# Kernel tuning notes

Hardware: AMD Instinct MI355X
Metric: run time of the kernel (lower is better)

Reference implementation:

```python
import jax, jax.numpy as jnp
import numpy as np

B, S, H, NH = 4, 2048, 1024, 16
D = H // NH  # head_dim = 64


def setup_inputs() -> dict:
    key = jax.random.key(0)
    ks = jax.random.split(key, 8)
    hidden_states = jax.random.normal(ks[0], (B, S, H), dtype=jnp.float32)
    attention_mask = jnp.zeros((B, 1, 1, S), dtype=jnp.float32)  # additive, bidirectional
    # RoPE tables (cos/sin per position, full head_dim)
    inv_freq = 1.0 / (10000.0 ** (jnp.arange(0, D, 2, dtype=jnp.float32) / D))
    t = jnp.arange(S, dtype=jnp.float32)
    freqs = jnp.outer(t, inv_freq)              # [S, D/2]
    emb = jnp.concatenate([freqs, freqs], -1)   # [S, D]
    cos, sin = jnp.cos(emb), jnp.sin(emb)
    scale = 1.0 / np.sqrt(H)
    Wq = jax.random.normal(ks[1], (H, H), dtype=jnp.float32) * scale
    Wk = jax.random.normal(ks[2], (H, H), dtype=jnp.float32) * scale
    Wv = jax.random.normal(ks[3], (H, H), dtype=jnp.float32) * scale
    Wo = jax.random.normal(ks[4], (H, H), dtype=jnp.float32) * scale
    return {"hidden_states": hidden_states, "attention_mask": attention_mask,
            "cos": cos, "sin": sin, "Wq": Wq, "Wk": Wk, "Wv": Wv, "Wo": Wo}


def _rotate_half(x):
    x1, x2 = jnp.split(x, 2, axis=-1)
    return jnp.concatenate([-x2, x1], axis=-1)


def _rope(x, cos, sin):
    # x: [B, NH, S, D]; cos/sin: [S, D]
    c = cos[None, None, :, :]
    s = sin[None, None, :, :]
    return x * c + _rotate_half(x) * s


def reference(hidden_states, attention_mask, cos, sin, Wq, Wk, Wv, Wo):
    b, s, h = hidden_states.shape
    # QKV projections (torch Linear: x @ W^T)
    def proj(W):
        y = jnp.einsum('bsh,oh->bso', hidden_states, W)
        return y.reshape(b, s, NH, D).transpose(0, 2, 1, 3)  # [B, NH, S, D]
    q, k, v = proj(Wq), proj(Wk), proj(Wv)
    q = _rope(q, cos, sin)
    k = _rope(k, cos, sin)
    scale = D ** -0.5
    scores = jnp.einsum('bhqd,bhkd->bhqk', q, k) * scale + attention_mask
    attn = jax.nn.softmax(scores, axis=-1)
    out = jnp.einsum('bhqk,bhkd->bhqd', attn, v)            # [B, NH, S, D]
    out = out.transpose(0, 2, 1, 3).reshape(b, s, h)        # [B, S, H]
    return jnp.einsum('bsh,oh->bso', out, Wo)
```

## Files before the change

kernel.cpp:

```cpp
#include <hip/hip_runtime.h>


typedef __bf16 bf16x8 __attribute__((ext_vector_type(8)));
typedef float f32x4 __attribute__((ext_vector_type(4)));
typedef float f32x16 __attribute__((ext_vector_type(16)));
typedef unsigned short u16x8 __attribute__((ext_vector_type(8)));
typedef unsigned short u16x4 __attribute__((ext_vector_type(4)));
typedef const __attribute__((address_space(1))) void* gptr_t;
typedef __attribute__((address_space(3))) void* lptr_t;

template <int N> struct ic { static constexpr int v = N; };

__device__ __forceinline__ unsigned short f2bf(float f) {
  union { float f; unsigned u; } v; v.f = f;
  unsigned r = (v.u + 0x7fffu + ((v.u >> 16) & 1u)) >> 16;
  return (unsigned short)r;
}

__device__ __forceinline__ unsigned short f2bfn(float f) {
  union { __bf16 h; unsigned short u; } v;
  v.h = (__bf16)f;
  return v.u;
}

__device__ __forceinline__ unsigned cvtpk(float lo, float hi_) {
  unsigned r;
  asm("v_cvt_pk_bf16_f32 %0, %1, %2" : "=v"(r) : "v"(lo), "v"(hi_));
  return r;
}

__device__ __forceinline__ void gld16(const void* g, void* l) {
  __builtin_amdgcn_global_load_lds((gptr_t)g, (lptr_t)l, 16, 0, 0);
}

__global__ __launch_bounds__(256) void cvt_all(
    const float* __restrict__ hidden, const float* __restrict__ Wq,
    const float* __restrict__ Wk, const float* __restrict__ Wv,
    const float* __restrict__ Wo, unsigned short* __restrict__ Xb,
    unsigned short* __restrict__ Wb) {
  size_t i8 = ((size_t)blockIdx.x * 256 + threadIdx.x) * 8;
  const float* src;
  unsigned short* dst;
  if (i8 < 8388608) {
    src = hidden + i8;
    dst = Xb + i8;
  } else {
    size_t r = i8 - 8388608;
    int wsel = (int)(r >> 20);
    size_t off = r & 1048575;
    const float* wsrc = (wsel == 0) ? Wq : (wsel == 1) ? Wk : (wsel == 2) ? Wv : Wo;
    src = wsrc + off;
    dst = Wb + r;
  }
  f32x4 a = *(const f32x4*)(src);
  f32x4 b = *(const f32x4*)(src + 4);
  u16x8 o;
  o[0] = f2bf(a[0]); o[1] = f2bf(a[1]); o[2] = f2bf(a[2]); o[3] = f2bf(a[3]);
  o[4] = f2bf(b[0]); o[5] = f2bf(b[1]); o[6] = f2bf(b[2]); o[7] = f2bf(b[3]);
  *(u16x8*)dst = o;
}

__global__ __launch_bounds__(768, 3) void gemm_qkv(
    const unsigned short* __restrict__ A,
    const unsigned short* __restrict__ W0, const unsigned short* __restrict__ W1,
    const unsigned short* __restrict__ W2,
    const float* __restrict__ cosT, const float* __restrict__ sinT,
    unsigned short* __restrict__ Qh, unsigned short* __restrict__ Kh,
    unsigned short* __restrict__ Vh) {
  __shared__ char sm[131072];
  const int tid = threadIdx.x, lane = tid & 63, w = tid >> 6;
  const int l15 = lane & 15, h2 = lane >> 4;
  const int z = w >> 2, sub = w & 3;
  const int wm = sub >> 1, wn = sub & 1;
  const int wg = blockIdx.x;
  const int work = (wg & 7) * 64 + (wg >> 3);
  const int bx = work & 7, by = work >> 3;
  const int brow = by * 128;
  const int bcol = bx * 128;

  const char* Abase = (const char*)A + (size_t)brow * 2048;
  const char* Wb0 = (const char*)W0 + (size_t)bcol * 2048;
  const char* Wb1 = (const char*)W1 + (size_t)bcol * 2048;
  const char* Wb2 = (const char*)W2 + (size_t)bcol * 2048;

  const char* gsrc[6];
  int gdst[6];
#pragma unroll
  for (int i = 0; i < 6; ++i) {
    int g = tid + i * 768;
    bool val = g < 4096;
    int gg = val ? g : 0;
    int r = (gg & 1023) >> 3;
    int sw = ((gg & 7) * 16) ^ ((r & 7) << 4);
    const char* base;
    if (gg < 1024) base = Abase;
    else {
      int zz = (gg >> 10) - 1;
      base = (zz == 0) ? Wb0 : (zz == 1 ? Wb1 : Wb2);
    }
    gsrc[i] = val ? (base + (size_t)r * 2048 + sw) : nullptr;
    gdst[i] = gg * 16;
  }

  f32x4 acc[4][4];
#pragma unroll
  for (int m = 0; m < 4; ++m)
#pragma unroll
    for (int n = 0; n < 4; ++n) acc[m][n] = (f32x4){0.f, 0.f, 0.f, 0.f};

#pragma unroll
  for (int i = 0; i < 6; ++i)
    if (gsrc[i]) gld16(gsrc[i], sm + gdst[i]);

  for (int kt = 0; kt < 16; ++kt) {
    const int cur = kt & 1, nxt = cur ^ 1;
    if (kt < 15) {
#pragma unroll
      for (int i = 0; i < 6; ++i)
        if (gsrc[i]) gld16(gsrc[i] + (kt + 1) * 128, sm + nxt * 65536 + gdst[i]);
      if (w < 4) asm volatile("s_waitcnt vmcnt(6)" ::: "memory");
      else       asm volatile("s_waitcnt vmcnt(5)" ::: "memory");
    } else {
      asm volatile("s_waitcnt vmcnt(0)" ::: "memory");
    }
    __builtin_amdgcn_sched_barrier(0);
    __builtin_amdgcn_s_barrier();
    __builtin_amdgcn_sched_barrier(0);

    const char* Asw = sm + cur * 65536;
    const char* Bsw = sm + cur * 65536 + 16384 + z * 16384;
#pragma unroll
    for (int kk = 0; kk < 2; ++kk) {
      int kb = kk * 64 + h2 * 16;
      bf16x8 af[4], bfr[4];
#pragma unroll
      for (int m = 0; m < 4; ++m) {
        int r = wm * 64 + m * 16 + l15;
        af[m] = *(const bf16x8*)(Asw + r * 128 + (kb ^ ((r & 7) << 4)));
      }
#pragma unroll
      for (int n = 0; n < 4; ++n) {
        int r = wn * 64 + n * 16 + l15;
        bfr[n] = *(const bf16x8*)(Bsw + r * 128 + (kb ^ ((r & 7) << 4)));
      }
#pragma unroll
      for (int m = 0; m < 4; ++m)
#pragma unroll
        for (int n = 0; n < 4; ++n)
          acc[m][n] = __builtin_amdgcn_mfma_f32_16x16x32_bf16(af[m], bfr[n],
                                                              acc[m][n], 0, 0, 0);
    }
    __builtin_amdgcn_sched_barrier(0);
    __builtin_amdgcn_s_barrier();
  }

  const int h = bx * 2 + wn;
  if (z == 2) {
#pragma unroll
    for (int m = 0; m < 4; ++m) {
      int row0 = brow + wm * 64 + m * 16 + h2 * 4;
      int b = row0 >> 11, s0 = row0 & 2047;
      size_t base = (size_t)(b * 16 + h) * 64 * 2048 + s0;
#pragma unroll
      for (int n = 0; n < 4; ++n) {
        int dl = n * 16 + l15;
        u16x4 pw;
#pragma unroll
        for (int i = 0; i < 4; ++i) pw[i] = f2bf(acc[m][n][i]);
        *(u16x4*)(Vh + base + (size_t)dl * 2048) = pw;
      }
    }
  } else {
    unsigned short* dst = (z == 0) ? Qh : Kh;
    const float qs = (z == 0) ? 0.18033688f : 1.0f;
#pragma unroll
    for (int m = 0; m < 4; ++m)
#pragma unroll
      for (int i = 0; i < 4; ++i) {
        int row = brow + wm * 64 + m * 16 + h2 * 4 + i;
        int b = row >> 11, s = row & 2047;
        size_t hb2 = ((size_t)(b * 16 + h) * 2048 + s) * 64;
#pragma unroll
        for (int n = 0; n < 2; ++n) {
          int dl = n * 16 + l15;
          float c = cosT[s * 64 + dl], sn = sinT[s * 64 + dl];
          float lo = acc[m][n][i], hi = acc[m][n + 2][i];
          dst[hb2 + dl] = f2bf((lo * c - hi * sn) * qs);
          dst[hb2 + dl + 32] = f2bf((hi * c + lo * sn) * qs);
        }
      }
  }
}

__global__ __launch_bounds__(256, 2) void gemm_k(
    const unsigned short* __restrict__ A, const unsigned short* __restrict__ W0,
    float* __restrict__ Cout) {
  __shared__ char sm[65536];
  const int tid = threadIdx.x, lane = tid & 63, w = tid >> 6;
  const int wm = w >> 1, wn = w & 1;
  const int wg = blockIdx.x;
  const int work = (wg & 7) * 64 + (wg >> 3);
  const int bx = work & 7, by = work >> 3;
  const int brow = by * 128;
  const int bcol = bx * 128;

  f32x4 acc[4][4];
#pragma unroll
  for (int m = 0; m < 4; ++m)
#pragma unroll
    for (int n = 0; n < 4; ++n) acc[m][n] = (f32x4){0.f, 0.f, 0.f, 0.f};

  const char* Abase = (const char*)A + (size_t)brow * 2048;
  const char* Bbase = (const char*)W0 + (size_t)bcol * 2048;

  const char* srcA[4];
  const char* srcB[4];
  int dstO[4];
#pragma unroll
  for (int c = 0; c < 4; ++c) {
    int Lb = w * 4096 + c * 1024;
    int L = Lb + lane * 16;
    int r = L >> 7, kb = L & 127;
    int sw = kb ^ ((r & 7) << 4);
    srcA[c] = Abase + (size_t)r * 2048 + sw;
    srcB[c] = Bbase + (size_t)r * 2048 + sw;
    dstO[c] = Lb;
  }

#pragma unroll
  for (int c = 0; c < 4; ++c) {
    gld16(srcA[c], sm + dstO[c]);
    gld16(srcB[c], sm + 16384 + dstO[c]);
  }

  for (int kt = 0; kt < 16; ++kt) {
    const int cur = kt & 1, nxt = cur ^ 1;
    if (kt < 15) {
#pragma unroll
      for (int c = 0; c < 4; ++c) {
        gld16(srcA[c] + (kt + 1) * 128, sm + nxt * 32768 + dstO[c]);
        gld16(srcB[c] + (kt + 1) * 128, sm + nxt * 32768 + 16384 + dstO[c]);
      }
      asm volatile("s_waitcnt vmcnt(8)" ::: "memory");
    } else {
      asm volatile("s_waitcnt vmcnt(0)" ::: "memory");
    }
    __builtin_amdgcn_sched_barrier(0);
    __builtin_amdgcn_s_barrier();
    __builtin_amdgcn_sched_barrier(0);

    const char* As = sm + cur * 32768;
    const char* Bs = sm + cur * 32768 + 16384;
#pragma unroll
    for (int kk = 0; kk < 2; ++kk) {
      int kb = kk * 64 + (lane >> 4) * 16;
      bf16x8 af[4], bfr[4];
#pragma unroll
      for (int m = 0; m < 4; ++m) {
        int r = wm * 64 + m * 16 + (lane & 15);
        af[m] = *(const bf16x8*)(As + r * 128 + (kb ^ ((r & 7) << 4)));
      }
#pragma unroll
      for (int n = 0; n < 4; ++n) {
        int r = wn * 64 + n * 16 + (lane & 15);
        bfr[n] = *(const bf16x8*)(Bs + r * 128 + (kb ^ ((r & 7) << 4)));
      }
#pragma unroll
      for (int m = 0; m < 4; ++m)
#pragma unroll
        for (int n = 0; n < 4; ++n)
          acc[m][n] = __builtin_amdgcn_mfma_f32_16x16x32_bf16(af[m], bfr[n],
                                                              acc[m][n], 0, 0, 0);
    }
    __builtin_amdgcn_sched_barrier(0);
    __builtin_amdgcn_s_barrier();
  }

#pragma unroll
  for (int m = 0; m < 4; ++m)
#pragma unroll
    for (int n = 0; n < 4; ++n)
#pragma unroll
      for (int i = 0; i < 4; ++i) {
        int row = brow + wm * 64 + m * 16 + (lane >> 4) * 4 + i;
        int col = bcol + wn * 64 + n * 16 + (lane & 15);
        Cout[(size_t)row * 1024 + col] = acc[m][n][i];
      }
}

__global__ __launch_bounds__(256, 4) void attn_k(
    const unsigned short* __restrict__ Q, const unsigned short* __restrict__ K,
    const unsigned short* __restrict__ Vt, const float* __restrict__ mask,
    unsigned short* __restrict__ O) {
  __shared__ char Ks[2][8192];
  __shared__ char Vs[2][8192];
  __shared__ float l_arr[4][32];
  const int tid = threadIdx.x, lane = tid & 63, w = tid >> 6;
  const int q31 = lane & 31, hi = lane >> 5;
  const int wg = blockIdx.x;
  const int work = (wg & 7) * 128 + (wg >> 3);
  const int qt = work & 15, hl = work >> 4;
  const int h = hl & 15, b = hl >> 4;
  const size_t hb = (size_t)(b * 16 + h) * (2048 * 64);
  const int q0 = qt * 128 + w * 32;
  const float L2E = 1.44269504f;
  const float MREF = 12.0f;
  const int rdo = q31 * 32 + hi * 16;

  bf16x8 qb[4];
  {
    const char* qrow = (const char*)(Q + hb + (size_t)(q0 + q31) * 64);
#pragma unroll
    for (int ks = 0; ks < 4; ++ks)
      qb[ks] = *(const bf16x8*)(qrow + ks * 32 + hi * 16);
  }

  float l_part = 0.f;
  f32x16 oacc[2];
#pragma unroll
  for (int e = 0; e < 16; ++e) { oacc[0][e] = 0.f; oacc[1][e] = 0.f; }

  int koff0, koff1, vof0, vof1;
  {
    int L0 = w * 2048 + lane * 16;
    int c0 = L0 >> 12, ks0 = (L0 >> 10) & 3, q0l = (L0 >> 5) & 31,
        hi0 = (L0 >> 4) & 1;
    int row0 = c0 * 32 + q0l, kb0 = ks0 * 32 + hi0 * 16;
    koff0 = row0 * 128 + kb0;
    vof0 = row0 * 4096 + kb0;
    int L1 = L0 + 1024;
    int c1 = L1 >> 12, ks1 = (L1 >> 10) & 3, q1l = (L1 >> 5) & 31,
        hi1 = (L1 >> 4) & 1;
    int row1 = c1 * 32 + q1l, kb1 = ks1 * 32 + hi1 * 16;
    koff1 = row1 * 128 + kb1;
    vof1 = row1 * 4096 + kb1;
  }
  const char* Kg = (const char*)(K + hb);
  const char* Vg = (const char*)(Vt + hb);
  const float* mp = mask + (size_t)b * 2048;

  gld16(Kg + koff0, Ks[0] + w * 2048);
  gld16(Kg + koff1, Ks[0] + w * 2048 + 1024);
  gld16(Vg + vof0, Vs[0] + w * 2048);
  gld16(Vg + vof1, Vs[0] + w * 2048 + 1024);

  auto body = [&](auto curc, int t) {
    constexpr int cur = decltype(curc)::v;
    constexpr int nxt = 1 - cur;
    if (t < 31) {
      const char* kp = Kg + (size_t)(t + 1) * 8192;
      const char* vp = Vg + (size_t)(t + 1) * 128;
      gld16(kp + koff0, Ks[nxt] + w * 2048);
      gld16(kp + koff1, Ks[nxt] + w * 2048 + 1024);
      gld16(vp + vof0, Vs[nxt] + w * 2048);
      gld16(vp + vof1, Vs[nxt] + w * 2048 + 1024);
      asm volatile("s_waitcnt vmcnt(4)" ::: "memory");
    } else {
      asm volatile("s_waitcnt vmcnt(0)" ::: "memory");
    }
    __builtin_amdgcn_sched_barrier(0);
    __builtin_amdgcn_s_barrier();
    __builtin_amdgcn_sched_barrier(0);

    const float* mrow = mp + t * 64;

    f32x16 sacc[2];
#pragma unroll
    for (int c = 0; c < 2; ++c) {
#pragma unroll
      for (int g = 0; g < 4; ++g) {
        f32x4 mv = *(const f32x4*)(mrow + c * 32 + g * 8 + hi * 4);
#pragma unroll
        for (int i = 0; i < 4; ++i)
          sacc[c][g * 4 + i] = fmaf(mv[i], L2E, -MREF);
      }
      __builtin_amdgcn_s_setprio(1);
#pragma unroll
      for (int ks = 0; ks < 4; ++ks) {
        bf16x8 kf =
            *(const bf16x8*)(Ks[cur] + (c * 4 + ks) * 1024 + rdo);
        sacc[c] = __builtin_amdgcn_mfma_f32_32x32x16_bf16(kf, qb[ks], sacc[c],
                                                          0, 0, 0);
      }
      __builtin_amdgcn_s_setprio(0);
#pragma unroll
      for (int e = 0; e < 16; ++e)
        sacc[c][e] = __builtin_amdgcn_exp2f(sacc[c][e]);
      float s0 = (sacc[c][0] + sacc[c][1]) + (sacc[c][2] + sacc[c][3]);
      float s1 = (sacc[c][4] + sacc[c][5]) + (sacc[c][6] + sacc[c][7]);
      float s2 = (sacc[c][8] + sacc[c][9]) + (sacc[c][10] + sacc[c][11]);
      float s3 = (sacc[c][12] + sacc[c][13]) + (sacc[c][14] + sacc[c][15]);
      l_part += (s0 + s1) + (s2 + s3);
    }

    __builtin_amdgcn_s_setprio(1);
#pragma unroll
    for (int c = 0; c < 2; ++c) {
#pragma unroll
      for (int par = 0; par < 2; ++par) {
        const int t2 = c * 2 + par;
        unsigned a0 = cvtpk(sacc[c][par * 8 + 0], sacc[c][par * 8 + 1]);
        unsigned a1 = cvtpk(sacc[c][par * 8 + 2], sacc[c][par * 8 + 3]);
        unsigned b0 = cvtpk(sacc[c][par * 8 + 4], sacc[c][par * 8 + 5]);
        unsigned b1 = cvtpk(sacc[c][par * 8 + 6], sacc[c][par * 8 + 7]);
        asm("v_permlane32_swap_b32 %0, %1" : "+v"(a0), "+v"(b0));
        asm("v_permlane32_swap_b32 %0, %1" : "+v"(a1), "+v"(b1));
        union { unsigned u[4]; bf16x8 v; } pu;
        pu.u[0] = a0; pu.u[1] = a1; pu.u[2] = b0; pu.u[3] = b1;
        bf16x8 vf0 = *(const bf16x8*)(Vs[cur] + t2 * 1024 + rdo);
        bf16x8 vf1 = *(const bf16x8*)(Vs[cur] + 4096 + t2 * 1024 + rdo);
        oacc[0] = __builtin_amdgcn_mfma_f32_32x32x16_bf16(pu.v, vf0, oacc[0],
                                                          0, 0, 0);
        oacc[1] = __builtin_amdgcn_mfma_f32_32x32x16_bf16(pu.v, vf1, oacc[1],
                                                          0, 0, 0);
      }
    }
    __builtin_amdgcn_s_setprio(0);
    __builtin_amdgcn_sched_barrier(0);
    __builtin_amdgcn_s_barrier();
  };

  for (int t = 0; t < 32; t += 2) {
    body(ic<0>{}, t);
    body(ic<1>{}, t + 1);
  }

  float lr = l_part + __shfl_xor(l_part, 32, 64);
  l_arr[w][q31] = 1.0f / lr;

#pragma unroll
  for (int g = 0; g < 4; ++g) {
    f32x4 iv = *(const f32x4*)(&l_arr[w][g * 8 + hi * 4]);
    const int qrow = q0 + g * 8 + hi * 4;
#pragma unroll
    for (int i = 0; i < 4; ++i) {
      size_t rb = (size_t)(b * 2048 + qrow + i) * 1024 + h * 64;
      O[rb + q31] = f2bfn(oacc[0][g * 4 + i] * iv[i]);
      O[rb + 32 + q31] = f2bfn(oacc[1][g * 4 + i] * iv[i]);
    }
  }
}

extern "C" void kernel_launch(void* const* d_in, const int* in_sizes, int n_in,
                              void* d_out, int out_size, void* d_ws, size_t ws_size,
                              hipStream_t stream) {
  const float* hidden = (const float*)d_in[0];
  const float* amask = (const float*)d_in[1];
  const float* cosT = (const float*)d_in[2];
  const float* sinT = (const float*)d_in[3];
  const float* Wq = (const float*)d_in[4];
  const float* Wk = (const float*)d_in[5];
  const float* Wv = (const float*)d_in[6];
  const float* Wo = (const float*)d_in[7];
  float* out = (float*)d_out;

  if (ws_size < (size_t)92274688) return;
  unsigned short* Xb = (unsigned short*)d_ws;
  unsigned short* Wqb = Xb + (size_t)8192 * 1024;
  unsigned short* Wkb = Wqb + (size_t)1024 * 1024;
  unsigned short* Wvb = Wkb + (size_t)1024 * 1024;
  unsigned short* Wob = Wvb + (size_t)1024 * 1024;
  unsigned short* Qh = Wob + (size_t)1024 * 1024;
  unsigned short* Kh = Qh + (size_t)8388608;
  unsigned short* Vt = Kh + (size_t)8388608;
  unsigned short* Ob = Vt + (size_t)8388608;

  cvt_all<<<6144, 256, 0, stream>>>(hidden, Wq, Wk, Wv, Wo, Xb, Wqb);

  gemm_qkv<<<512, 768, 0, stream>>>(Xb, Wqb, Wkb, Wvb, cosT, sinT, Qh, Kh, Vt);
  attn_k<<<1024, 256, 0, stream>>>(Qh, Kh, Vt, amask, Ob);
  gemm_k<<<512, 256, 0, stream>>>(Ob, Wob, out);
}
```

Before: 191.6 us.

## Software-pipeline attention loop: compute next tile's QK^T while exponentiating current

Restructures the attention inner loop so that the QK^T MFMAs for tile t+1 are issued alongside the exp2/pack softmax work of tile t, with K prefetched two tiles ahead and V one tile ahead. The goal is to overlap MFMA execution with the VALU exp and convert work, which previously ran one after the other. In exchange it holds two sets of score accumulators live, which raises VGPR pressure, and the buffer indexing and waitcnt logic become more complex.

```diff
diff --git a/kernel.cpp b/kernel.cpp
--- a/kernel.cpp
+++ b/kernel.cpp
@@ -10,6 +10,7 @@
 typedef __attribute__((address_space(3))) void* lptr_t;
 
 template <int N> struct ic { static constexpr int v = N; };
+struct pu4 { unsigned u[4]; };
 
 __device__ __forceinline__ unsigned short f2bf(float f) {
   union { float f; unsigned u; } v; v.f = f;
@@ -339,81 +340,101 @@
   const char* Vg = (const char*)(Vt + hb);
   const float* mp = mask + (size_t)b * 2048;
 
+  auto qkc = [&](const char* ksb, const float* mrow, int c) -> f32x16 {
+    f32x16 s;
+#pragma unroll
+    for (int g = 0; g < 4; ++g) {
+      f32x4 mv = *(const f32x4*)(mrow + c * 32 + g * 8 + hi * 4);
+#pragma unroll
+      for (int i = 0; i < 4; ++i) s[g * 4 + i] = fmaf(mv[i], L2E, -MREF);
+    }
+    __builtin_amdgcn_s_setprio(1);
+#pragma unroll
+    for (int ks = 0; ks < 4; ++ks) {
+      bf16x8 kf = *(const bf16x8*)(ksb + (c * 4 + ks) * 1024 + rdo);
+      s = __builtin_amdgcn_mfma_f32_32x32x16_bf16(kf, qb[ks], s, 0, 0, 0);
+    }
+    __builtin_amdgcn_s_setprio(0);
+    return s;
+  };
+
+  auto smpack = [&](f32x16& s, pu4& pa, pu4& pb) {
+#pragma unroll
+    for (int e = 0; e < 16; ++e) s[e] = __builtin_amdgcn_exp2f(s[e]);
+    l_part += ((s[0] + s[1]) + (s[2] + s[3])) + ((s[4] + s[5]) + (s[6] + s[7])) +
+              ((s[8] + s[9]) + (s[10] + s[11])) +
+              ((s[12] + s[13]) + (s[14] + s[15]));
+#pragma unroll
+    for (int par = 0; par < 2; ++par) {
+      unsigned a0 = cvtpk(s[par * 8 + 0], s[par * 8 + 1]);
+      unsigned a1 = cvtpk(s[par * 8 + 2], s[par * 8 + 3]);
+      unsigned b0 = cvtpk(s[par * 8 + 4], s[par * 8 + 5]);
+      unsigned b1 = cvtpk(s[par * 8 + 6], s[par * 8 + 7]);
+      asm("v_permlane32_swap_b32 %0, %1" : "+v"(a0), "+v"(b0));
+      asm("v_permlane32_swap_b32 %0, %1" : "+v"(a1), "+v"(b1));
+      pu4& pp = par ? pb : pa;
+      pp.u[0] = a0; pp.u[1] = a1; pp.u[2] = b0; pp.u[3] = b1;
+    }
+  };
+
   gld16(Kg + koff0, Ks[0] + w * 2048);
   gld16(Kg + koff1, Ks[0] + w * 2048 + 1024);
   gld16(Vg + vof0, Vs[0] + w * 2048);
   gld16(Vg + vof1, Vs[0] + w * 2048 + 1024);
-
-  auto body = [&](auto curc, int t) {
-    constexpr int cur = decltype(curc)::v;
-    constexpr int nxt = 1 - cur;
+  gld16(Kg + 8192 + koff0, Ks[1] + w * 2048);
+  gld16(Kg + 8192 + koff1, Ks[1] + w * 2048 + 1024);
+  asm volatile("s_waitcnt vmcnt(2)" ::: "memory");
+  __builtin_amdgcn_sched_barrier(0);
+  __builtin_amdgcn_s_barrier();
+  __builtin_amdgcn_sched_barrier(0);
+
+  f32x16 sA0, sA1, sB0, sB1;
+  sA0 = qkc(Ks[0], mp, 0);
+  sA1 = qkc(Ks[0], mp, 1);
+  __builtin_amdgcn_sched_barrier(0);
+  __builtin_amdgcn_s_barrier();
+
+  auto body = [&](auto vbc, int t, f32x16& sP0, f32x16& sP1, f32x16& sN0,
+                  f32x16& sN1) {
+    constexpr int vb = decltype(vbc)::v;
+    constexpr int kb1 = 1 - vb;
+    if (t < 30) {
+      const char* kp = Kg + (size_t)(t + 2) * 8192;
+      gld16(kp + koff0, Ks[vb] + w * 2048);
+      gld16(kp + koff1, Ks[vb] + w * 2048 + 1024);
+    }
     if (t < 31) {
-      const char* kp = Kg + (size_t)(t + 1) * 8192;
       const char* vp = Vg + (size_t)(t + 1) * 128;
-      gld16(kp + koff0, Ks[nxt] + w * 2048);
-      gld16(kp + koff1, Ks[nxt] + w * 2048 + 1024);
-      gld16(vp + vof0, Vs[nxt] + w * 2048);
-      gld16(vp + vof1, Vs[nxt] + w * 2048 + 1024);
-      asm volatile("s_waitcnt vmcnt(4)" ::: "memory");
-    } else {
-      asm volatile("s_waitcnt vmcnt(0)" ::: "memory");
-    }
-    __builtin_amdgcn_sched_barrier(0);
-    __builtin_amdgcn_s_barrier();
-    __builtin_amdgcn_sched_barrier(0);
-
-    const float* mrow = mp + t * 64;
-
-    f32x16 sacc[2];
-#pragma unroll
-    for (int c = 0; c < 2; ++c) {
-#pragma unroll
-      for (int g = 0; g < 4; ++g) {
-        f32x4 mv = *(const f32x4*)(mrow + c * 32 + g * 8 + hi * 4);
-#pragma unroll
-        for (int i = 0; i < 4; ++i)
-          sacc[c][g * 4 + i] = fmaf(mv[i], L2E, -MREF);
-      }
-      __builtin_amdgcn_s_setprio(1);
-#pragma unroll
-      for (int ks = 0; ks < 4; ++ks) {
-        bf16x8 kf =
-            *(const bf16x8*)(Ks[cur] + (c * 4 + ks) * 1024 + rdo);
-        sacc[c] = __builtin_amdgcn_mfma_f32_32x32x16_bf16(kf, qb[ks], sacc[c],
-                                                          0, 0, 0);
-      }
-      __builtin_amdgcn_s_setprio(0);
-#pragma unroll
-      for (int e = 0; e < 16; ++e)
-        sacc[c][e] = __builtin_amdgcn_exp2f(sacc[c][e]);
-      float s0 = (sacc[c][0] + sacc[c][1]) + (sacc[c][2] + sacc[c][3]);
-      float s1 = (sacc[c][4] + sacc[c][5]) + (sacc[c][6] + sacc[c][7]);
-      float s2 = (sacc[c][8] + sacc[c][9]) + (sacc[c][10] + sacc[c][11]);
-      float s3 = (sacc[c][12] + sacc[c][13]) + (sacc[c][14] + sacc[c][15]);
-      l_part += (s0 + s1) + (s2 + s3);
-    }
+      gld16(vp + vof0, Vs[kb1] + w * 2048);
+      gld16(vp + vof1, Vs[kb1] + w * 2048 + 1024);
+    }
+    if (t < 30) asm volatile("s_waitcnt vmcnt(4)" ::: "memory");
+    else if (t < 31) asm volatile("s_waitcnt vmcnt(2)" ::: "memory");
+    else asm volatile("s_waitcnt vmcnt(0)" ::: "memory");
+    __builtin_amdgcn_sched_barrier(0);
+    __builtin_amdgcn_s_barrier();
+    __builtin_amdgcn_sched_barrier(0);
+
+    const float* mnext = mp + (t + 1) * 64;
+    pu4 p0, p1, p2, p3;
+    if (t < 31) sN0 = qkc(Ks[kb1], mnext, 0);
+    smpack(sP0, p0, p1);
+    if (t < 31) sN1 = qkc(Ks[kb1], mnext, 1);
+    smpack(sP1, p2, p3);
 
     __builtin_amdgcn_s_setprio(1);
 #pragma unroll
-    for (int c = 0; c < 2; ++c) {
-#pragma unroll
-      for (int par = 0; par < 2; ++par) {
-        const int t2 = c * 2 + par;
-        unsigned a0 = cvtpk(sacc[c][par * 8 + 0], sacc[c][par * 8 + 1]);
-        unsigned a1 = cvtpk(sacc[c][par * 8 + 2], sacc[c][par * 8 + 3]);
-        unsigned b0 = cvtpk(sacc[c][par * 8 + 4], sacc[c][par * 8 + 5]);
-        unsigned b1 = cvtpk(sacc[c][par * 8 + 6], sacc[c][par * 8 + 7]);
-        asm("v_permlane32_swap_b32 %0, %1" : "+v"(a0), "+v"(b0));
-        asm("v_permlane32_swap_b32 %0, %1" : "+v"(a1), "+v"(b1));
-        union { unsigned u[4]; bf16x8 v; } pu;
-        pu.u[0] = a0; pu.u[1] = a1; pu.u[2] = b0; pu.u[3] = b1;
-        bf16x8 vf0 = *(const bf16x8*)(Vs[cur] + t2 * 1024 + rdo);
-        bf16x8 vf1 = *(const bf16x8*)(Vs[cur] + 4096 + t2 * 1024 + rdo);
-        oacc[0] = __builtin_amdgcn_mfma_f32_32x32x16_bf16(pu.v, vf0, oacc[0],
-                                                          0, 0, 0);
-        oacc[1] = __builtin_amdgcn_mfma_f32_32x32x16_bf16(pu.v, vf1, oacc[1],
-                                                          0, 0, 0);
-      }
+    for (int t2 = 0; t2 < 4; ++t2) {
+      const pu4& pp = (t2 == 0) ? p0 : (t2 == 1) ? p1 : (t2 == 2) ? p2 : p3;
+      union { unsigned u[4]; bf16x8 v; } puv;
+      puv.u[0] = pp.u[0]; puv.u[1] = pp.u[1];
+      puv.u[2] = pp.u[2]; puv.u[3] = pp.u[3];
+      bf16x8 vf0 = *(const bf16x8*)(Vs[vb] + t2 * 1024 + rdo);
+      bf16x8 vf1 = *(const bf16x8*)(Vs[vb] + 4096 + t2 * 1024 + rdo);
+      oacc[0] = __builtin_amdgcn_mfma_f32_32x32x16_bf16(puv.v, vf0, oacc[0],
+                                                        0, 0, 0);
+      oacc[1] = __builtin_amdgcn_mfma_f32_32x32x16_bf16(puv.v, vf1, oacc[1],
+                                                        0, 0, 0);
     }
     __builtin_amdgcn_s_setprio(0);
     __builtin_amdgcn_sched_barrier(0);
@@ -421,8 +442,8 @@
   };
 
   for (int t = 0; t < 32; t += 2) {
-    body(ic<0>{}, t);
-    body(ic<1>{}, t + 1);
+    body(ic<0>{}, t, sA0, sA1, sB0, sB1);
+    body(ic<1>{}, t + 1, sB0, sB1, sA0, sA1);
   }
 
   float lr = l_part + __shfl_xor(l_part, 32, 64);
```

Result: slower. 642.3 us (+235.3%).
